# Kernel optimization log

Measured on AMD Instinct MI355X. Metric: run time of the kernel, lower is better.

Reference implementation:

```python
import jax, jax.numpy as jnp
import numpy as np

N_NODES = 50000


def gcn_conv(x, W, b, src, dst):
    # PyG GCNConv: h = x @ W; add self-loops; norm = deg^{-1/2}[src]*deg^{-1/2}[dst];
    # out = scatter_add(norm * h[src] -> dst) + bias
    h = x @ W  # [N, out]
    ones = jnp.ones(src.shape[0], dtype=x.dtype)
    deg = jax.ops.segment_sum(ones, dst, num_segments=N_NODES) + 1.0  # +1 for self-loop
    inv_sqrt = deg ** -0.5
    norm = inv_sqrt[src] * inv_sqrt[dst]  # [E]
    msgs = h[src] * norm[:, None]  # [E, out]
    agg = jax.ops.segment_sum(msgs, dst, num_segments=N_NODES)
    # self-loop contribution: norm_ii = deg_i^{-1}
    agg = agg + h * (inv_sqrt * inv_sqrt)[:, None]
    return agg + b


def setup_inputs() -> dict:
    key = jax.random.key(0)
    k1, k2, k3, k4 = jax.random.split(key, 4)
    d_in, d_h = 256, 256
    x = jax.random.normal(k1, (N_NODES, d_in), dtype=jnp.float32)
    edge_index = jax.random.randint(k2, (2, 800000), 0, N_NODES, dtype=jnp.int64)
    # Glorot-style params (GCNConv linear has no bias; separate bias added post-agg)
    W1 = jax.random.normal(k3, (d_in, d_h), dtype=jnp.float32) / np.sqrt(d_in)
    W2 = jax.random.normal(k4, (d_h, d_h), dtype=jnp.float32) / np.sqrt(d_h)
    b1 = jnp.zeros((d_h,), dtype=jnp.float32)
    b2 = jnp.zeros((d_h,), dtype=jnp.float32)
    return {"x": x, "edge_index": edge_index, "W1": W1, "b1": b1, "W2": W2, "b2": b2}


def reference(x, edge_index, W1, b1, W2, b2):
    src, dst = edge_index[0], edge_index[1]
    h = jax.nn.relu(gcn_conv(x, W1, b1, src, dst))
    h = jax.nn.relu(gcn_conv(h, W2, b2, src, dst))
    # global_mean_pool with batch=arange(N) assigns each node its own graph -> identity
    return h
```

## Files before the change

### kernel.cpp

```cpp
#include <hip/hip_runtime.h>
#include <hip/hip_bf16.h>

typedef unsigned short u16;
typedef unsigned int u32;

#define N_NODES 50000
#define N_EDGES 800000
#define DHID 256
#define ELLW 64

typedef __attribute__((ext_vector_type(8))) _Float16 f16x8;
typedef __attribute__((ext_vector_type(4))) float f32x4;
typedef __attribute__((ext_vector_type(2))) float f32x2;

__device__ __forceinline__ u16 f2bf(float f) {
    u32 u = __float_as_uint(f);
    u32 r = (u + 0x7FFFu + ((u >> 16) & 1u)) >> 16;
    return (u16)r;
}
__device__ __forceinline__ u16 f2h(float f) {
    _Float16 h = (_Float16)f;
    union { _Float16 h; u16 u; } c; c.h = h;
    return c.u;
}
__device__ __forceinline__ void gl_lds16(const void* g, void* l) {
    __builtin_amdgcn_global_load_lds(
        (const __attribute__((address_space(1))) u32*)g,
        (__attribute__((address_space(3))) u32*)l, 16, 0, 0);
}

#define SPLIT_BLKS 12500
#define ZERO_BLKS 196
__global__ void prep_fused(const float* __restrict__ x, u16* __restrict__ xf,
                           const float* __restrict__ W1, const float* __restrict__ W2,
                           u16* __restrict__ W1t, u16* __restrict__ W2t,
                           int* __restrict__ deg, u32* __restrict__ hszero) {
    const int b = blockIdx.x, tid = threadIdx.x;
    if (b < SPLIT_BLKS) {
        int i = b * 256 + tid;
        float4 v = ((const float4*)x)[i];
        u16 h0 = f2h(v.x), h1 = f2h(v.y), h2 = f2h(v.z), h3 = f2h(v.w);
        uint2 hv;
        hv.x = (u32)h0 | ((u32)h1 << 16);
        hv.y = (u32)h2 | ((u32)h3 << 16);
        ((uint2*)xf)[i] = hv;
    } else if (b < SPLIT_BLKS + ZERO_BLKS) {
        int j = (b - SPLIT_BLKS) * 256 + tid;
        if (j < N_NODES) deg[j] = 0;
        if (j < 128) hszero[j] = 0;
    } else {
        int idx = b - (SPLIT_BLKS + ZERO_BLKS);
        int y = idx >> 8, n = idx & 255, k = tid;
        const float* W = y ? W2 : W1;
        u16* o = y ? W2t : W1t;
        o[n * 256 + k] = f2h(W[k * 256 + n]);
    }
}

__global__ void fill_kernel(const int* __restrict__ src, const int* __restrict__ dst,
                            int* __restrict__ deg, u16* __restrict__ col16, int E) {
    int e = blockIdx.x * 256 + threadIdx.x;
    if (e < E) {
        int d = dst[e];
        int p = atomicAdd(&deg[d], 1);
        if (p < ELLW) col16[(size_t)d * ELLW + p] = (u16)src[e];
    }
}

__global__ __launch_bounds__(256) void gemm_f16_kernel(
    const u16* __restrict__ Af, const u16* __restrict__ Bt,
    const int* __restrict__ deg, u16* __restrict__ out, int M) {
    __shared__ u16 As[128 * 32];
    __shared__ u16 Bs[128 * 32];
    const int tid = threadIdx.x;
    const int wave = tid >> 6;
    const int lane = tid & 63;
    const int wm = wave >> 1, wn = wave & 1;
    const int quad = lane >> 4, l16 = lane & 15;
    const int m0 = blockIdx.x * 128;
    const int n0 = blockIdx.y * 128;

    f32x4 acc[4][4] = {};

    const int row0 = tid >> 2, row1 = (256 + tid) >> 2;
    const int kk = (tid & 3) * 8;
    int ar0 = m0 + row0; if (ar0 >= M) ar0 = M - 1;
    int ar1 = m0 + row1; if (ar1 >= M) ar1 = M - 1;
    const size_t aoff0 = (size_t)ar0 * 256 + kk;
    const size_t aoff1 = (size_t)ar1 * 256 + kk;
    const size_t boff0 = (size_t)(n0 + row0) * 256 + kk;
    const size_t boff1 = (size_t)(n0 + row1) * 256 + kk;
    const size_t l0 = (size_t)(wave * 64) * 8;
    const size_t l1 = (size_t)(256 + wave * 64) * 8;

    for (int ko = 0; ko < 8; ++ko) {
        const int koff = ko * 32;
        __syncthreads();
        gl_lds16(Af + aoff0 + koff, &As[l0]);
        gl_lds16(Af + aoff1 + koff, &As[l1]);
        gl_lds16(Bt + boff0 + koff, &Bs[l0]);
        gl_lds16(Bt + boff1 + koff, &Bs[l1]);
        asm volatile("s_waitcnt vmcnt(0)" ::: "memory");
        __syncthreads();

        f16x8 af[4], bf[4];
#pragma unroll
        for (int mi = 0; mi < 4; ++mi)
            af[mi] = *(const f16x8*)&As[(wm * 64 + mi * 16 + l16) * 32 + quad * 8];
#pragma unroll
        for (int ni = 0; ni < 4; ++ni)
            bf[ni] = *(const f16x8*)&Bs[(wn * 64 + ni * 16 + l16) * 32 + quad * 8];
#pragma unroll
        for (int mi = 0; mi < 4; ++mi)
#pragma unroll
            for (int ni = 0; ni < 4; ++ni)
                acc[mi][ni] = __builtin_amdgcn_mfma_f32_16x16x32_f16(af[mi], bf[ni], acc[mi][ni], 0, 0, 0);
    }

#pragma unroll
    for (int mi = 0; mi < 4; ++mi) {
#pragma unroll
        for (int r = 0; r < 4; ++r) {
            int row = m0 + wm * 64 + mi * 16 + quad * 4 + r;
            if (row < M) {
                float s = rsqrtf((float)deg[row] + 1.0f);
#pragma unroll
                for (int ni = 0; ni < 4; ++ni) {
                    int c = n0 + wn * 64 + ni * 16 + l16;
                    out[(size_t)row * 256 + c] = f2bf(acc[mi][ni][r] * s);
                }
            }
        }
    }
}

__global__ __launch_bounds__(256) void agg_kernel(
    const u16* __restrict__ hs, const u16* __restrict__ col16,
    const int* __restrict__ deg, const float* __restrict__ bias,
    u16* __restrict__ out_f16, float* __restrict__ out_f,
    int mode, int Nn) {
    const int wave = threadIdx.x >> 6, lane = threadIdx.x & 63;
    const int i = blockIdx.x * 4 + wave;
    if (i >= Nn) return;

    const int cnt = deg[i];
    const size_t ebase = (size_t)i * ELLW;
    int entry = Nn;
    if (lane == 0) entry = i;
    else if (lane - 1 < cnt) entry = (int)col16[ebase + lane - 1];
    int entries = cnt + 1;
    if (entries > 64) entries = 64;
    const int nb = (entries + 3) >> 2;
    const size_t lofs = (size_t)lane * 4;

    f32x2 a01 = {0.f, 0.f}, a23 = {0.f, 0.f};

#define ISSUE(b, x0, x1, x2, x3)                                                \
    {                                                                           \
        int e0 = __builtin_amdgcn_readlane(entry, (b) * 4 + 0);                 \
        int e1 = __builtin_amdgcn_readlane(entry, (b) * 4 + 1);                 \
        int e2 = __builtin_amdgcn_readlane(entry, (b) * 4 + 2);                 \
        int e3 = __builtin_amdgcn_readlane(entry, (b) * 4 + 3);                 \
        x0 = *(const uint2*)(hs + (size_t)e0 * 256 + lofs);                     \
        x1 = *(const uint2*)(hs + (size_t)e1 * 256 + lofs);                     \
        x2 = *(const uint2*)(hs + (size_t)e2 * 256 + lofs);                     \
        x3 = *(const uint2*)(hs + (size_t)e3 * 256 + lofs);                     \
    }
#define ACCUM(v)                                                                \
    {                                                                           \
        f32x2 p0, p1;                                                           \
        p0.x = __uint_as_float(v.x << 16);                                      \
        p0.y = __uint_as_float(v.x & 0xffff0000u);                              \
        p1.x = __uint_as_float(v.y << 16);                                      \
        p1.y = __uint_as_float(v.y & 0xffff0000u);                              \
        a01 += p0; a23 += p1;                                                   \
    }

    uint2 c0, c1, c2, c3, d0, d1, d2, d3, n0v, n1v, n2v, n3v;
    ISSUE(0, c0, c1, c2, c3);
    if (nb > 1) ISSUE(1, d0, d1, d2, d3);
    for (int b = 0; b < nb; ++b) {
        const bool more2 = (b + 2 < nb);
        if (more2) ISSUE(b + 2, n0v, n1v, n2v, n3v);
        ACCUM(c0); ACCUM(c1); ACCUM(c2); ACCUM(c3);
        c0 = d0; c1 = d1; c2 = d2; c3 = d3;
        d0 = n0v; d1 = n1v; d2 = n2v; d3 = n3v;
    }
    {
        int cap = cnt < ELLW ? cnt : ELLW;
        for (int j = 63; j < cap; ++j) {
            int s = (int)col16[ebase + j];
            uint2 v = *(const uint2*)(hs + (size_t)s * 256 + lofs);
            ACCUM(v);
        }
    }
#undef ISSUE
#undef ACCUM

    const float inv = rsqrtf((float)cnt + 1.0f);
    float4 bb = *(const float4*)(bias + lane * 4);
    float r0 = fmaxf(fmaf(a01.x, inv, bb.x), 0.0f);
    float r1 = fmaxf(fmaf(a01.y, inv, bb.y), 0.0f);
    float r2 = fmaxf(fmaf(a23.x, inv, bb.z), 0.0f);
    float r3 = fmaxf(fmaf(a23.y, inv, bb.w), 0.0f);
    const size_t o = (size_t)i * 256 + lane * 4;
    if (mode == 0) {
        u16 h0 = f2h(r0), h1 = f2h(r1), h2 = f2h(r2), h3 = f2h(r3);
        uint2 w;
        w.x = (u32)h0 | ((u32)h1 << 16);
        w.y = (u32)h2 | ((u32)h3 << 16);
        *(uint2*)(out_f16 + o) = w;
    } else {
        *(float4*)(out_f + o) = make_float4(r0, r1, r2, r3);
    }
}

extern "C" void kernel_launch(void* const* d_in, const int* in_sizes, int n_in,
                              void* d_out, int out_size, void* d_ws, size_t ws_size,
                              hipStream_t stream) {
    const float* x = (const float*)d_in[0];
    const int* ei = (const int*)d_in[1];
    const float* W1 = (const float*)d_in[2];
    const float* b1 = (const float*)d_in[3];
    const float* W2 = (const float*)d_in[4];
    const float* b2 = (const float*)d_in[5];
    float* out = (float*)d_out;

    const int Nn = N_NODES, E = N_EDGES;
    const int* srcp = ei;
    const int* dstp = ei + E;

    u16* Af = (u16*)d_out;

    char* p = (char*)d_ws;
    auto take = [&](size_t bytes) -> void* {
        void* r = (void*)p;
        p += (bytes + 255) & ~(size_t)255;
        return r;
    };
    u16* hs    = (u16*)take((size_t)(Nn + 1) * DHID * 2);
    u16* col16 = (u16*)take((size_t)Nn * ELLW * 2);
    int* deg   = (int*)take((size_t)Nn * 4);
    u16* W1t   = (u16*)take(256 * 256 * 2);
    u16* W2t   = (u16*)take(256 * 256 * 2);

    prep_fused<<<SPLIT_BLKS + ZERO_BLKS + 512, 256, 0, stream>>>(
        x, Af, W1, W2, W1t, W2t, deg, (u32*)(hs + (size_t)Nn * DHID));
    fill_kernel<<<E / 256, 256, 0, stream>>>(srcp, dstp, deg, col16, E);

    const int gm = (Nn + 127) / 128;
    gemm_f16_kernel<<<dim3(gm, 2), 256, 0, stream>>>(Af, W1t, deg, hs, Nn);
    agg_kernel<<<(Nn + 3) / 4, 256, 0, stream>>>(hs, col16, deg, b1, Af, nullptr, 0, Nn);
    gemm_f16_kernel<<<dim3(gm, 2), 256, 0, stream>>>(Af, W2t, deg, hs, Nn);
    agg_kernel<<<(Nn + 3) / 4, 256, 0, stream>>>(hs, col16, deg, b2, nullptr, out, 1, Nn);
}
```

Before: 305.1 us.

## Split prep kernel, batch fill atomics, split agg launches, move Af to workspace

Splits the fused prep kernel into a zero/weight-transpose kernel and a separate x-to-f16 conversion kernel. The ELL fill kernel now handles 8 edges per thread, issuing all loads first and then all atomics, so more memory operations are in flight. Each aggregation is split into two half-range launches, and the f16 activation buffer moves from the output buffer into workspace when space allows. The net effect is several unrelated tweaks that add extra kernel launches and their overhead.

```diff
diff --git a/kernel.cpp b/kernel.cpp
--- a/kernel.cpp
+++ b/kernel.cpp
@@ -29,27 +29,16 @@
         (__attribute__((address_space(3))) u32*)l, 16, 0, 0);
 }
 
-#define SPLIT_BLKS 12500
-#define ZERO_BLKS 196
-__global__ void prep_fused(const float* __restrict__ x, u16* __restrict__ xf,
-                           const float* __restrict__ W1, const float* __restrict__ W2,
-                           u16* __restrict__ W1t, u16* __restrict__ W2t,
-                           int* __restrict__ deg, u32* __restrict__ hszero) {
+__global__ void zero_w_kernel(int* __restrict__ deg, u32* __restrict__ hs32,
+                              const float* __restrict__ W1, const float* __restrict__ W2,
+                              u16* __restrict__ W1t, u16* __restrict__ W2t) {
     const int b = blockIdx.x, tid = threadIdx.x;
-    if (b < SPLIT_BLKS) {
-        int i = b * 256 + tid;
-        float4 v = ((const float4*)x)[i];
-        u16 h0 = f2h(v.x), h1 = f2h(v.y), h2 = f2h(v.z), h3 = f2h(v.w);
-        uint2 hv;
-        hv.x = (u32)h0 | ((u32)h1 << 16);
-        hv.y = (u32)h2 | ((u32)h3 << 16);
-        ((uint2*)xf)[i] = hv;
-    } else if (b < SPLIT_BLKS + ZERO_BLKS) {
-        int j = (b - SPLIT_BLKS) * 256 + tid;
+    if (b < 196) {
+        int j = b * 256 + tid;
         if (j < N_NODES) deg[j] = 0;
-        if (j < 128) hszero[j] = 0;
+        if (j < 128) hs32[(size_t)N_NODES * 128 + j] = 0;
     } else {
-        int idx = b - (SPLIT_BLKS + ZERO_BLKS);
+        int idx = b - 196;
         int y = idx >> 8, n = idx & 255, k = tid;
         const float* W = y ? W2 : W1;
         u16* o = y ? W2t : W1t;
@@ -57,14 +46,35 @@
     }
 }
 
+#define SPLIT_BLKS 12500
+__global__ void prep_kernel(const float* __restrict__ x, u16* __restrict__ xf) {
+    int i = blockIdx.x * 256 + threadIdx.x;
+    float4 v = ((const float4*)x)[i];
+    uint2 hv;
+    hv.x = (u32)f2h(v.x) | ((u32)f2h(v.y) << 16);
+    hv.y = (u32)f2h(v.z) | ((u32)f2h(v.w) << 16);
+    ((uint2*)xf)[i] = hv;
+}
+
+#define FILL_BLKS 391
 __global__ void fill_kernel(const int* __restrict__ src, const int* __restrict__ dst,
-                            int* __restrict__ deg, u16* __restrict__ col16, int E) {
-    int e = blockIdx.x * 256 + threadIdx.x;
-    if (e < E) {
-        int d = dst[e];
-        int p = atomicAdd(&deg[d], 1);
-        if (p < ELLW) col16[(size_t)d * ELLW + p] = (u16)src[e];
-    }
+                            int* __restrict__ deg, u16* __restrict__ col16) {
+    const int tid = threadIdx.x;
+    const int e0 = blockIdx.x * 2048 + tid;
+    int ds[8], ps[8], ss[8];
+    bool ok[8];
+#pragma unroll
+    for (int q = 0; q < 8; ++q) {
+        int e = e0 + q * 256;
+        ok[q] = (e < N_EDGES);
+        if (ok[q]) { ds[q] = dst[e]; ss[q] = src[e]; }
+    }
+#pragma unroll
+    for (int q = 0; q < 8; ++q)
+        if (ok[q]) ps[q] = atomicAdd(&deg[ds[q]], 1);
+#pragma unroll
+    for (int q = 0; q < 8; ++q)
+        if (ok[q] && ps[q] < ELLW) col16[(size_t)ds[q] * ELLW + ps[q]] = (u16)ss[q];
 }
 
 __global__ __launch_bounds__(256) void gemm_f16_kernel(
@@ -138,9 +148,9 @@
     const u16* __restrict__ hs, const u16* __restrict__ col16,
     const int* __restrict__ deg, const float* __restrict__ bias,
     u16* __restrict__ out_f16, float* __restrict__ out_f,
-    int mode, int Nn) {
+    int mode, int off, int Nn) {
     const int wave = threadIdx.x >> 6, lane = threadIdx.x & 63;
-    const int i = blockIdx.x * 4 + wave;
+    const int i = off + blockIdx.x * 4 + wave;
     if (i >= Nn) return;
 
     const int cnt = deg[i];
@@ -230,8 +240,6 @@
     const int* srcp = ei;
     const int* dstp = ei + E;
 
-    u16* Af = (u16*)d_out;
-
     char* p = (char*)d_ws;
     auto take = [&](size_t bytes) -> void* {
         void* r = (void*)p;
@@ -243,14 +251,20 @@
     int* deg   = (int*)take((size_t)Nn * 4);
     u16* W1t   = (u16*)take(256 * 256 * 2);
     u16* W2t   = (u16*)take(256 * 256 * 2);
-
-    prep_fused<<<SPLIT_BLKS + ZERO_BLKS + 512, 256, 0, stream>>>(
-        x, Af, W1, W2, W1t, W2t, deg, (u32*)(hs + (size_t)Nn * DHID));
-    fill_kernel<<<E / 256, 256, 0, stream>>>(srcp, dstp, deg, col16, E);
+    size_t used = (size_t)(p - (char*)d_ws);
+    size_t af_bytes = (size_t)Nn * DHID * 2;
+    u16* Af = (ws_size >= used + af_bytes) ? (u16*)take(af_bytes) : (u16*)d_out;
+
+    zero_w_kernel<<<708, 256, 0, stream>>>(deg, (u32*)hs, W1, W2, W1t, W2t);
+    prep_kernel<<<SPLIT_BLKS, 256, 0, stream>>>(x, Af);
+    fill_kernel<<<FILL_BLKS, 256, 0, stream>>>(srcp, dstp, deg, col16);
 
     const int gm = (Nn + 127) / 128;
+    const int gah = 6250;
     gemm_f16_kernel<<<dim3(gm, 2), 256, 0, stream>>>(Af, W1t, deg, hs, Nn);
-    agg_kernel<<<(Nn + 3) / 4, 256, 0, stream>>>(hs, col16, deg, b1, Af, nullptr, 0, Nn);
+    agg_kernel<<<gah, 256, 0, stream>>>(hs, col16, deg, b1, Af, nullptr, 0, 0, Nn);
+    agg_kernel<<<gah, 256, 0, stream>>>(hs, col16, deg, b1, Af, nullptr, 0, 25000, Nn);
     gemm_f16_kernel<<<dim3(gm, 2), 256, 0, stream>>>(Af, W2t, deg, hs, Nn);
-    agg_kernel<<<(Nn + 3) / 4, 256, 0, stream>>>(hs, col16, deg, b2, nullptr, out, 1, Nn);
-}
+    agg_kernel<<<gah, 256, 0, stream>>>(hs, col16, deg, b2, nullptr, out, 1, 0, Nn);
+    agg_kernel<<<gah, 256, 0, stream>>>(hs, col16, deg, b2, nullptr, out, 1, 25000, Nn);
+}
```

Result: slower. 315.3 us (+3.3%).
